# Kernel tuning notes

Measured on AMD Instinct MI355X. Metric: run time of the kernel, lower is better.

Reference implementation:

```python
import jax, jax.numpy as jnp
import numpy as np

F_DIM = 49   # kernel / input frequency extent
T_DIM = 25   # kernel time extent
C_OUT, C_IN, G = 16, 1, 4


def _build_kernel(W, P, SIG):
    # DCLS ConstructKernel2d, version='gauss'.
    # P: (2, C_out, C_in, G) offsets; shifted by (F//2, T//2) to kernel coords.
    # SIG: (2, C_out, C_in, G); sigma = |SIG| + 0.27.
    dt = W.dtype
    mu_f = P[0] + jnp.asarray(F_DIM // 2, dt)          # (O,I,G)
    mu_t = P[1] + jnp.asarray(T_DIM // 2, dt)
    sig = jnp.abs(SIG) + jnp.asarray(0.27, dt)
    f = jnp.arange(F_DIM, dtype=dt)                    # (F,)
    t = jnp.arange(T_DIM, dtype=dt)                    # (T,)
    df = (f[:, None, None, None] - mu_f) / sig[0]      # (F,O,I,G)
    dtt = (t[:, None, None, None] - mu_t) / sig[1]     # (T,O,I,G)
    # squared 2-norm of ((IDX - P)/SIG) over the 2 spatial axes
    X = jnp.exp(-0.5 * (df[:, None] ** 2 + dtt[None, :] ** 2))  # (F,T,O,I,G)
    X = X / (X.sum(axis=(0, 1), keepdims=True) + jnp.asarray(1e-7, dt))
    K = jnp.einsum('ftoig,oig->oift', X, W)            # (O,I,F,T)
    return K


def setup_inputs() -> dict:
    key = jax.random.key(0)
    k1, k2, k3, k4, k5 = jax.random.split(key, 5)
    x = jax.random.normal(k1, (64, C_IN, F_DIM, 8000), dtype=jnp.float32)
    W = jax.random.normal(k2, (C_OUT, C_IN, G), dtype=jnp.float32) * 0.5
    p_f = jax.random.uniform(k3, (C_OUT, C_IN, G), minval=-F_DIM / 2, maxval=F_DIM / 2)
    p_t = jax.random.uniform(k4, (C_OUT, C_IN, G), minval=-T_DIM / 2, maxval=T_DIM / 2)
    P = jnp.stack([p_f, p_t], axis=0).astype(jnp.float32)          # (2,O,I,G)
    SIG = (0.1 + 0.4 * jax.random.uniform(k5, (2, C_OUT, C_IN, G))).astype(jnp.float32)
    return {"x": x, "W": W, "P": P, "SIG": SIG}


def reference(x, W, P, SIG):
    K = _build_kernel(W, P, SIG)
    # causal pad on time (last) dim: (T-1, 0)
    xp = jnp.pad(x, ((0, 0), (0, 0), (0, 0), (T_DIM - 1, 0)))
    out = jax.lax.conv_general_dilated(
        xp, K, window_strides=(1, 1), padding='VALID',
        dimension_numbers=('NCHW', 'OIHW', 'NCHW'))
    return out  # (B, C_out, F_in - F + 1, T_in)
```

## Files before the change

kernel.cpp:

```cpp
#include <hip/hip_runtime.h>
#include <math.h>

#define F_DIM 49
#define T_DIM 25
#define O_CH  16
#define G_CH  4
#define OG    64
#define T_IN  8000
#define B_SZ  64

__global__ void strf_prep(const float* __restrict__ W,
                          const float* __restrict__ P,
                          const float* __restrict__ SIG,
                          float* __restrict__ Kf,
                          float* __restrict__ Kt)
{
    int og = threadIdx.x;
    if (og >= OG) return;
    float mu_f = P[og]      + (float)(F_DIM / 2);
    float mu_t = P[OG + og] + (float)(T_DIM / 2);
    float sf = fabsf(SIG[og])      + 0.27f;
    float st = fabsf(SIG[OG + og]) + 0.27f;

    float xf[F_DIM];
    float Sf = 0.0f;
#pragma unroll
    for (int f = 0; f < F_DIM; ++f) {
        float d = ((float)f - mu_f) / sf;
        float e = expf(-0.5f * d * d);
        xf[f] = e;
        Sf += e;
    }
    float xt[T_DIM];
    float St = 0.0f;
#pragma unroll
    for (int t = 0; t < T_DIM; ++t) {
        float d = ((float)t - mu_t) / st;
        float e = expf(-0.5f * d * d);
        xt[t] = e;
        St += e;
    }
    float scale = W[og] / (Sf * St + 1e-7f);
#pragma unroll
    for (int f = 0; f < F_DIM; ++f) Kf[f * OG + og] = xf[f];
#pragma unroll
    for (int t = 0; t < T_DIM; ++t) Kt[og * T_DIM + t] = xt[t] * scale;
}

__global__ __launch_bounds__(256)
void strf_freq(const float* __restrict__ x,
               const float* __restrict__ Kf,
               float* __restrict__ yf,
               int b0)
{
    const int chunk = blockIdx.x * 256 + threadIdx.x;
    const int bl    = blockIdx.y;
    const int og0   = blockIdx.z * 16;
    if (chunk >= T_IN / 4) return;
    const int tau0 = chunk * 4;

    const float* xp = x + (size_t)(b0 + bl) * (F_DIM * T_IN) + tau0;

    float acc[16][4];
#pragma unroll
    for (int i = 0; i < 16; ++i)
#pragma unroll
        for (int j = 0; j < 4; ++j) acc[i][j] = 0.0f;

    float4 cur = *(const float4*)xp;
#pragma unroll 2
    for (int f = 0; f < F_DIM - 1; ++f) {
        float4 nxt = *(const float4*)(xp + (size_t)(f + 1) * T_IN);
        const float* kfp = Kf + f * OG + og0;
        float4 k0 = *(const float4*)(kfp);
        float4 k1 = *(const float4*)(kfp + 4);
        float4 k2 = *(const float4*)(kfp + 8);
        float4 k3 = *(const float4*)(kfp + 12);
        float kv[16] = {k0.x, k0.y, k0.z, k0.w, k1.x, k1.y, k1.z, k1.w,
                        k2.x, k2.y, k2.z, k2.w, k3.x, k3.y, k3.z, k3.w};
        float cv[4] = {cur.x, cur.y, cur.z, cur.w};
#pragma unroll
        for (int i = 0; i < 16; ++i)
#pragma unroll
            for (int j = 0; j < 4; ++j)
                acc[i][j] = fmaf(kv[i], cv[j], acc[i][j]);
        cur = nxt;
    }
    {
        const float* kfp = Kf + (F_DIM - 1) * OG + og0;
        float4 k0 = *(const float4*)(kfp);
        float4 k1 = *(const float4*)(kfp + 4);
        float4 k2 = *(const float4*)(kfp + 8);
        float4 k3 = *(const float4*)(kfp + 12);
        float kv[16] = {k0.x, k0.y, k0.z, k0.w, k1.x, k1.y, k1.z, k1.w,
                        k2.x, k2.y, k2.z, k2.w, k3.x, k3.y, k3.z, k3.w};
        float cv[4] = {cur.x, cur.y, cur.z, cur.w};
#pragma unroll
        for (int i = 0; i < 16; ++i)
#pragma unroll
            for (int j = 0; j < 4; ++j)
                acc[i][j] = fmaf(kv[i], cv[j], acc[i][j]);
    }

    float* yp = yf + ((size_t)bl * OG + og0) * T_IN + tau0;
#pragma unroll
    for (int i = 0; i < 16; ++i)
        *(float4*)(yp + (size_t)i * T_IN) =
            make_float4(acc[i][0], acc[i][1], acc[i][2], acc[i][3]);
}

__global__ __launch_bounds__(256)
void strf_time(const float* __restrict__ yf,
               const float* __restrict__ Kt,
               float* __restrict__ out,
               int b0)
{
    const int chunk = blockIdx.x * 256 + threadIdx.x;
    if (chunk >= T_IN / 8) return;
    const int o    = blockIdx.y;
    const int bl   = blockIdx.z;
    const int tau0 = chunk * 8;

    float acc[8];
#pragma unroll
    for (int j = 0; j < 8; ++j) acc[j] = 0.0f;

#pragma unroll
    for (int g = 0; g < G_CH; ++g) {
        const int og = o * G_CH + g;
        const float* ktp = Kt + og * T_DIM;
        float kt[T_DIM];
#pragma unroll
        for (int t = 0; t < T_DIM; ++t) kt[t] = ktp[t];

        const float* yp = yf + ((size_t)bl * OG + og) * T_IN;
        float w[32];
        if (tau0 >= 24) {
            const float* base = yp + tau0 - 24;
#pragma unroll
            for (int j = 0; j < 8; ++j) {
                float4 v = *(const float4*)(base + 4 * j);
                w[4 * j + 0] = v.x; w[4 * j + 1] = v.y;
                w[4 * j + 2] = v.z; w[4 * j + 3] = v.w;
            }
        } else {
#pragma unroll
            for (int m = 0; m < 32; ++m) {
                int t = tau0 - 24 + m;
                w[m] = (t >= 0) ? yp[t] : 0.0f;
            }
        }
#pragma unroll
        for (int t = 0; t < T_DIM; ++t)
#pragma unroll
            for (int j = 0; j < 8; ++j)
                acc[j] = fmaf(kt[t], w[t + j], acc[j]);
    }

    float* op = out + ((size_t)(b0 + bl) * O_CH + o) * T_IN + tau0;
    *(float4*)op       = make_float4(acc[0], acc[1], acc[2], acc[3]);
    *(float4*)(op + 4) = make_float4(acc[4], acc[5], acc[6], acc[7]);
}

#define TILE  128
#define EXT   160
#define XSW   168
#define YFW   176

__global__ __launch_bounds__(256, 2)
void strf_main(const float* __restrict__ x,
               const float* __restrict__ Kf,
               const float* __restrict__ Kt,
               float* __restrict__ out)
{
    __shared__ __align__(16) float xs[F_DIM * XSW];
    __shared__ __align__(16) float yfs[OG * YFW];

    const int tid  = threadIdx.x;
    const int tile = blockIdx.x;
    const int b    = blockIdx.y;
    const int t0   = tile * TILE;

    const float* xb = x + (size_t)b * (F_DIM * T_IN);
    for (int idx = tid; idx < F_DIM * EXT; idx += 256) {
        int f = idx / EXT;
        int c = idx - f * EXT;
        int tg = t0 - (T_DIM - 1) + c;
        float v = (tg >= 0 && tg < T_IN) ? xb[f * T_IN + tg] : 0.0f;
        xs[f * XSW + c] = v;
    }
    __syncthreads();

    {
        const int og0  = (tid >> 5) * 8;
        const int tg   = tid & 31;
        const int tau0 = tg * 5;

        float acc[8][5];
#pragma unroll
        for (int i = 0; i < 8; ++i)
#pragma unroll
            for (int j = 0; j < 5; ++j) acc[i][j] = 0.0f;

        const float* kfp = Kf + og0;
        const float* xsp = xs + tau0;
        for (int f = 0; f < F_DIM; ++f) {
            float xv[5];
#pragma unroll
            for (int j = 0; j < 5; ++j) xv[j] = xsp[j];
            xsp += XSW;
            float4 k0 = *(const float4*)(kfp);
            float4 k1 = *(const float4*)(kfp + 4);
            kfp += OG;
            float kf[8] = {k0.x, k0.y, k0.z, k0.w, k1.x, k1.y, k1.z, k1.w};
#pragma unroll
            for (int i = 0; i < 8; ++i)
#pragma unroll
                for (int j = 0; j < 5; ++j)
                    acc[i][j] = fmaf(kf[i], xv[j], acc[i][j]);
        }
#pragma unroll
        for (int i = 0; i < 8; ++i) {
            float* row = yfs + (og0 + i) * YFW;
#pragma unroll
            for (int j = 0; j < 5; ++j) {
                int c  = tau0 + j;
                int pc = c + ((c >> 5) << 2);
                row[pc] = acc[i][j];
            }
        }
    }
    __syncthreads();

    {
        const int o    = tid >> 4;
        const int tg   = tid & 15;
        const int tau0 = tg * 8;

        float acc[8];
#pragma unroll
        for (int j = 0; j < 8; ++j) acc[j] = 0.0f;

        for (int g = 0; g < G_CH; ++g) {
            const int og = o * G_CH + g;
            float kt[T_DIM];
            const float* ktp = Kt + og * T_DIM;
#pragma unroll
            for (int t = 0; t < T_DIM; ++t) kt[t] = ktp[t];

            float w[32];
            const float* row = yfs + og * YFW;
#pragma unroll
            for (int ch = 0; ch < 8; ++ch) {
                int c  = tau0 + ch * 4;
                int pc = c + ((c >> 5) << 2);
                float4 v = *(const float4*)(row + pc);
                w[ch * 4 + 0] = v.x;
                w[ch * 4 + 1] = v.y;
                w[ch * 4 + 2] = v.z;
                w[ch * 4 + 3] = v.w;
            }
#pragma unroll
            for (int t = 0; t < T_DIM; ++t)
#pragma unroll
                for (int j = 0; j < 8; ++j)
                    acc[j] = fmaf(kt[t], w[t + j], acc[j]);
        }

        const int taug = t0 + tau0;
        if (taug + 7 < T_IN) {
            float* op = out + ((size_t)b * O_CH + o) * T_IN + taug;
            *(float4*)op       = make_float4(acc[0], acc[1], acc[2], acc[3]);
            *(float4*)(op + 4) = make_float4(acc[4], acc[5], acc[6], acc[7]);
        }
    }
}

extern "C" void kernel_launch(void* const* d_in, const int* in_sizes, int n_in,
                              void* d_out, int out_size, void* d_ws, size_t ws_size,
                              hipStream_t stream) {
    const float* x   = (const float*)d_in[0];
    const float* W   = (const float*)d_in[1];
    const float* P   = (const float*)d_in[2];
    const float* SIG = (const float*)d_in[3];
    float* outp = (float*)d_out;

    float* Kf = (float*)d_ws;
    float* Kt = Kf + F_DIM * OG;

    strf_prep<<<dim3(1), dim3(64), 0, stream>>>(W, P, SIG, Kf, Kt);

    const size_t yf_off_b  = 32768;
    const size_t per_b     = (size_t)OG * T_IN * sizeof(float);
    const size_t avail     = (ws_size > yf_off_b) ? (ws_size - yf_off_b) : 0;
    const int    max_nb    = (int)(avail / per_b);

    if (max_nb >= 8) {
        float* yfp = (float*)((char*)d_ws + yf_off_b);
        for (int b0 = 0; b0 < B_SZ; ) {
            int nb = B_SZ - b0;
            if (nb > max_nb) nb = max_nb;
            strf_freq<<<dim3((T_IN / 4 + 255) / 256, nb, G_CH),
                        dim3(256), 0, stream>>>(x, Kf, yfp, b0);
            strf_time<<<dim3((T_IN / 8 + 255) / 256, O_CH, nb),
                        dim3(256), 0, stream>>>(yfp, Kt, outp, b0);
            b0 += nb;
        }
    } else {
        dim3 grid((T_IN + TILE - 1) / TILE, B_SZ);
        strf_main<<<grid, dim3(256), 0, stream>>>(x, Kf, Kt, outp);
    }
}
```

Baseline: 250.0 us.

## Store frequency-stage intermediate as bf16 and stage time-conv windows in LDS

The intermediate yf produced by the frequency pass is now written as bf16 instead of fp32, which halves its global write and read traffic and lets larger batch chunks fit in the workspace. The time-convolution kernel is rewritten to load a 2000-sample segment plus a 24-sample halo for all four Gaussian groups into shared memory. Each thread then reads its 32-sample window from there and unpacks the bf16 values to fp32. This trades accuracy in the intermediate for bandwidth, and about 6 of 256 threads exit after the cooperative load.

```diff
diff --git a/kernel.cpp b/kernel.cpp
--- a/kernel.cpp
+++ b/kernel.cpp
@@ -8,6 +8,22 @@
 #define OG    64
 #define T_IN  8000
 #define B_SZ  64
+#define SEG   2000
+#define HALO  24
+#define LW    (SEG + HALO)
+#define LSTR  2032
+
+typedef unsigned int  uint32;
+typedef unsigned short ushort16;
+
+__device__ __forceinline__ ushort16 f2bf(float x) {
+    uint32 u = __float_as_uint(x);
+    u = (u + 0x7fffu + ((u >> 16) & 1u)) >> 16;
+    return (ushort16)u;
+}
+__device__ __forceinline__ float bf2f(ushort16 h) {
+    return __uint_as_float(((uint32)h) << 16);
+}
 
 __global__ void strf_prep(const float* __restrict__ W,
                           const float* __restrict__ P,
@@ -50,7 +66,7 @@
 __global__ __launch_bounds__(256)
 void strf_freq(const float* __restrict__ x,
                const float* __restrict__ Kf,
-               float* __restrict__ yf,
+               ushort16* __restrict__ yf,
                int b0)
 {
     const int chunk = blockIdx.x * 256 + threadIdx.x;
@@ -102,24 +118,42 @@
                 acc[i][j] = fmaf(kv[i], cv[j], acc[i][j]);
     }
 
-    float* yp = yf + ((size_t)bl * OG + og0) * T_IN + tau0;
-#pragma unroll
-    for (int i = 0; i < 16; ++i)
-        *(float4*)(yp + (size_t)i * T_IN) =
-            make_float4(acc[i][0], acc[i][1], acc[i][2], acc[i][3]);
+    ushort16* yp = yf + ((size_t)bl * OG + og0) * T_IN + tau0;
+#pragma unroll
+    for (int i = 0; i < 16; ++i) {
+        ushort4 v;
+        v.x = f2bf(acc[i][0]); v.y = f2bf(acc[i][1]);
+        v.z = f2bf(acc[i][2]); v.w = f2bf(acc[i][3]);
+        *(ushort4*)(yp + (size_t)i * T_IN) = v;
+    }
 }
 
 __global__ __launch_bounds__(256)
-void strf_time(const float* __restrict__ yf,
-               const float* __restrict__ Kt,
-               float* __restrict__ out,
-               int b0)
+void strf_time2(const ushort16* __restrict__ yf,
+                const float* __restrict__ Kt,
+                float* __restrict__ out,
+                int b0)
 {
-    const int chunk = blockIdx.x * 256 + threadIdx.x;
-    if (chunk >= T_IN / 8) return;
-    const int o    = blockIdx.y;
-    const int bl   = blockIdx.z;
-    const int tau0 = chunk * 8;
+    __shared__ __align__(16) ushort16 ys[G_CH * LSTR];
+
+    const int tid = threadIdx.x;
+    const int seg = blockIdx.x;
+    const int o   = blockIdx.y;
+    const int bl  = blockIdx.z;
+
+    const ushort16* yg = yf + ((size_t)bl * OG + o * G_CH) * T_IN;
+    const int tbase = seg * SEG - HALO;
+    for (int e = tid; e < G_CH * LW; e += 256) {
+        int r = e / LW;
+        int c = e - r * LW;
+        int tg = tbase + c;
+        ys[r * LSTR + c] = (tg >= 0) ? yg[(size_t)r * T_IN + tg] : (ushort16)0;
+    }
+    __syncthreads();
+
+    const int chunk = tid;
+    if (chunk >= SEG / 8) return;
+    const int tau0 = seg * SEG + chunk * 8;
 
     float acc[8];
 #pragma unroll
@@ -127,29 +161,28 @@
 
 #pragma unroll
     for (int g = 0; g < G_CH; ++g) {
-        const int og = o * G_CH + g;
-        const float* ktp = Kt + og * T_DIM;
+        const float* ktp = Kt + (o * G_CH + g) * T_DIM;
         float kt[T_DIM];
 #pragma unroll
         for (int t = 0; t < T_DIM; ++t) kt[t] = ktp[t];
 
-        const float* yp = yf + ((size_t)bl * OG + og) * T_IN;
+        const uint4* p = (const uint4*)&ys[g * LSTR + chunk * 8];
+        uint4 a = p[0], b = p[1];
+        uint32 uw[8] = {a.x, a.y, a.z, a.w, b.x, b.y, b.z, b.w};
         float w[32];
-        if (tau0 >= 24) {
-            const float* base = yp + tau0 - 24;
-#pragma unroll
-            for (int j = 0; j < 8; ++j) {
-                float4 v = *(const float4*)(base + 4 * j);
-                w[4 * j + 0] = v.x; w[4 * j + 1] = v.y;
-                w[4 * j + 2] = v.z; w[4 * j + 3] = v.w;
-            }
-        } else {
-#pragma unroll
-            for (int m = 0; m < 32; ++m) {
-                int t = tau0 - 24 + m;
-                w[m] = (t >= 0) ? yp[t] : 0.0f;
-            }
-        }
+#pragma unroll
+        for (int k = 0; k < 8; ++k) {
+            w[2 * k + 0] = __uint_as_float(uw[k] << 16);
+            w[2 * k + 1] = __uint_as_float(uw[k] & 0xffff0000u);
+        }
+        uint4 c2 = p[2], d2 = p[3];
+        uint32 uw2[8] = {c2.x, c2.y, c2.z, c2.w, d2.x, d2.y, d2.z, d2.w};
+#pragma unroll
+        for (int k = 0; k < 8; ++k) {
+            w[16 + 2 * k + 0] = __uint_as_float(uw2[k] << 16);
+            w[16 + 2 * k + 1] = __uint_as_float(uw2[k] & 0xffff0000u);
+        }
+
 #pragma unroll
         for (int t = 0; t < T_DIM; ++t)
 #pragma unroll
@@ -291,19 +324,19 @@
     strf_prep<<<dim3(1), dim3(64), 0, stream>>>(W, P, SIG, Kf, Kt);
 
     const size_t yf_off_b  = 32768;
-    const size_t per_b     = (size_t)OG * T_IN * sizeof(float);
+    const size_t per_b     = (size_t)OG * T_IN * sizeof(ushort16);
     const size_t avail     = (ws_size > yf_off_b) ? (ws_size - yf_off_b) : 0;
     const int    max_nb    = (int)(avail / per_b);
 
     if (max_nb >= 8) {
-        float* yfp = (float*)((char*)d_ws + yf_off_b);
+        ushort16* yfp = (ushort16*)((char*)d_ws + yf_off_b);
         for (int b0 = 0; b0 < B_SZ; ) {
             int nb = B_SZ - b0;
             if (nb > max_nb) nb = max_nb;
             strf_freq<<<dim3((T_IN / 4 + 255) / 256, nb, G_CH),
                         dim3(256), 0, stream>>>(x, Kf, yfp, b0);
-            strf_time<<<dim3((T_IN / 8 + 255) / 256, O_CH, nb),
-                        dim3(256), 0, stream>>>(yfp, Kt, outp, b0);
+            strf_time2<<<dim3(T_IN / SEG, O_CH, nb),
+                         dim3(256), 0, stream>>>(yfp, Kt, outp, b0);
             b0 += nb;
         }
     } else {
```

After: 235.8 us. 1.06x faster.
